# Performance work log

Measured on AMD Instinct MI355X. Metric: run time of the kernel, lower is better.

The kernel has to match this reference:

```python
import jax, jax.numpy as jnp
import numpy as np

N_NODES = 50000
IN_DIM = 128
N_HID = 128
K = 4
ROUTIT = 3
N_LAYER = 2
TAU = 1.0


def setup_inputs() -> dict:
    key = jax.random.key(0)
    k1, k2, k3, k4, k5, k6 = jax.random.split(key, 6)
    feat = jax.random.normal(k1, (N_NODES, IN_DIM), dtype=jnp.float32)
    edge_index = jax.random.randint(k2, (2, 800000), 0, N_NODES, dtype=jnp.int64)
    # nn.Linear-style params (stored as [in, out] for x @ W + b)
    lin_w = jax.random.normal(k3, (IN_DIM, N_HID), dtype=jnp.float32) / np.sqrt(IN_DIM)
    lin_b = jax.random.normal(k4, (N_HID,), dtype=jnp.float32) * 0.01
    mlp_w = jax.random.normal(k5, (N_HID, N_HID), dtype=jnp.float32) / np.sqrt(N_HID)
    mlp_b = jax.random.normal(k6, (N_HID,), dtype=jnp.float32) * 0.01
    return {"feat": feat, "edge_index": edge_index, "lin_w": lin_w,
            "lin_b": lin_b, "mlp_w": mlp_w, "mlp_b": mlp_b}


def _channel_normalize(x, n, k, dd):
    # F.normalize over each of the k channels (eps matches torch default 1e-12)
    v = x.reshape(n, k, dd)
    nrm = jnp.linalg.norm(v, axis=2, keepdims=True)
    return (v / jnp.maximum(nrm, 1e-12)).reshape(n, k * dd)


def _routing_layer(x, src, trg):
    n, d = x.shape
    m = src.shape[0]
    dd = d // K
    x = _channel_normalize(x, n, K, dd)
    z = x[src].reshape(m, K, dd)  # gather per-edge source features
    c = x
    for t in range(ROUTIT):
        # Faithful to torch: c[trg].view(m, dd, K) is a reshape, NOT a transpose.
        # matmul(z, c_reshaped).sum(-1) == einsum over dd with c_reshaped summed over its trailing K.
        s = c[trg].reshape(m, dd, K).sum(axis=-1)          # [m, dd]
        p = jnp.einsum('mka,ma->mk', z, s)                 # [m, K]
        p = jax.nn.softmax(p / TAU, axis=1)
        weight_sum = (p[:, :, None] * z).reshape(m, d)     # [m, d]
        c = jax.ops.segment_sum(weight_sum, trg, num_segments=n) + x
        if t < ROUTIT - 1:
            c = _channel_normalize(c, n, K, dd)
    return c


def reference(feat, edge_index, lin_w, lin_b, mlp_w, mlp_b):
    src = edge_index[0]
    trg = edge_index[1]
    x = feat @ lin_w + lin_b
    for _ in range(N_LAYER):
        x = _routing_layer(x, src, trg)
    out = x @ mlp_w + mlp_b
    return (out, x)
```

## Files before the change

### kernel.cpp

```cpp
#include <hip/hip_runtime.h>

#define NN 50000
#define ND (NN * 128)
#define SCAN_B 49
#define CAP 20
#define LOG2E 1.4426950408889634f

typedef float f32x2 __attribute__((ext_vector_type(2)));

#if defined(__has_builtin)
#  if __has_builtin(__builtin_amdgcn_exp2f)
#    define EXP2F(x) __builtin_amdgcn_exp2f(x)
#  else
#    define EXP2F(x) exp2f(x)
#  endif
#else
#  define EXP2F(x) exp2f(x)
#endif

__device__ __forceinline__ float b2f(unsigned short u) {
    union { unsigned int i; float f; } v; v.i = ((unsigned int)u) << 16; return v.f;
}
__device__ __forceinline__ unsigned short f2b(float f) {
    union { float f; unsigned int i; } v; v.f = f;
    return (unsigned short)((v.i + 0x7fffu + ((v.i >> 16) & 1u)) >> 16);
}
__device__ __forceinline__ unsigned int pack2(float lo, float hi) {
    return (unsigned int)f2b(lo) | ((unsigned int)f2b(hi) << 16);
}
__device__ __forceinline__ float unlo(unsigned int u) { return __uint_as_float(u << 16); }
__device__ __forceinline__ float unhi(unsigned int u) { return __uint_as_float(u & 0xFFFF0000u); }
__device__ __forceinline__ int clampi(int i, int lo, int hi) { return max(lo, min(i, hi)); }

template<int CTRL>
__device__ __forceinline__ float dmov(float v) {
    return __int_as_float(__builtin_amdgcn_update_dpp(0, __float_as_int(v), CTRL, 0xF, 0xF, true));
}
template<int CTRL> __device__ __forceinline__ float dadd(float v) { return v + dmov<CTRL>(v); }
__device__ __forceinline__ float qsum(float v) { v = dadd<0xB1>(v); v = dadd<0x4E>(v); return v; }
__device__ __forceinline__ float rsum4(float v) { v = dadd<0x124>(v); v = dadd<0x128>(v); return v; }

__global__ __launch_bounds__(256) void detect(
    const unsigned short* __restrict__ feat_u, const unsigned int* __restrict__ ei_u,
    int* __restrict__ flags)
{
    int tid = threadIdx.x;
    int f32hit = 0;
    for (int i = tid; i < 8192; i += 256) {
        unsigned e = (feat_u[i] >> 7) & 0xFFu;
        if (e >= 0xC0u) f32hit = 1;
    }
    int i32hit = 0;
    for (int i = tid; i < 4096; i += 256)
        if (ei_u[2 * i + 1] != 0u) i32hit = 1;
    if (f32hit) atomicOr(&flags[0], 1);
    if (i32hit) atomicOr(&flags[1], 1);
}

__global__ __launch_bounds__(256) void conv_hist(
    const void* __restrict__ eiRaw, int* __restrict__ srcA, int* __restrict__ trgA,
    int* __restrict__ deg, int m, const int* __restrict__ flags)
{
    int e = blockIdx.x * 256 + threadIdx.x;
    if (e >= m) return;
    int src, trg;
    if (flags[1]) { const int* p = (const int*)eiRaw; src = p[e]; trg = p[m + e]; }
    else { const long long* p = (const long long*)eiRaw; src = (int)p[e]; trg = (int)p[m + e]; }
    src = clampi(src, 0, NN - 1);
    trg = clampi(trg, 0, NN - 1);
    srcA[e] = src; trgA[e] = trg;
    atomicAdd(&deg[trg], 1);
}

__global__ __launch_bounds__(256) void scan1(
    const int* __restrict__ deg, int* __restrict__ rowStart, int* __restrict__ blkSum)
{
    __shared__ int lds[256];
    int blk = blockIdx.x, tid = threadIdx.x;
    int base = blk * 1024 + tid * 4;
    int v[4]; int s = 0;
    #pragma unroll
    for (int j = 0; j < 4; ++j) { int idx = base + j; v[j] = (idx < NN) ? deg[idx] : 0; s += v[j]; }
    lds[tid] = s; __syncthreads();
    for (int off = 1; off < 256; off <<= 1) {
        int x = (tid >= off) ? lds[tid - off] : 0;
        __syncthreads();
        lds[tid] += x;
        __syncthreads();
    }
    int excl = lds[tid] - s;
    if (tid == 255) blkSum[blk] = lds[tid];
    int run = excl;
    #pragma unroll
    for (int j = 0; j < 4; ++j) { int idx = base + j; if (idx < NN) rowStart[idx] = run; run += v[j]; }
}
__global__ __launch_bounds__(64) void scan2(
    int* __restrict__ blkSum, int* __restrict__ blkOff, int* __restrict__ rowStart, int m)
{
    int lane = threadIdx.x;
    int orig = (lane < SCAN_B) ? blkSum[lane] : 0;
    int v = orig;
    for (int off = 1; off < 64; off <<= 1) {
        int x = __shfl_up(v, off);
        if (lane >= off) v += x;
    }
    if (lane < SCAN_B) blkOff[lane] = v - orig;
    if (lane == 0) rowStart[NN] = m;
}
__global__ __launch_bounds__(256) void scan3(
    int* __restrict__ rowStart, const int* __restrict__ blkOff, int* __restrict__ cursor)
{
    int base = blockIdx.x * 1024 + threadIdx.x * 4;
    int off = blkOff[blockIdx.x];
    #pragma unroll
    for (int j = 0; j < 4; ++j) {
        int idx = base + j;
        if (idx < NN) { int v = rowStart[idx] + off; rowStart[idx] = v; cursor[idx] = v; }
    }
}

__global__ __launch_bounds__(256) void scatter_csr(
    const int* __restrict__ srcA, const int* __restrict__ trgA,
    int* __restrict__ cursor, int* __restrict__ eSrc, int m)
{
    int e = blockIdx.x * 256 + threadIdx.x;
    if (e >= m) return;
    int pos = atomicAdd(&cursor[trgA[e]], 1);
    eSrc[pos] = srcA[e];
}

__global__ __launch_bounds__(256) void gemm_norm(
    const void* __restrict__ A, const void* __restrict__ W, const void* __restrict__ bias,
    unsigned short* __restrict__ XNh, const int* __restrict__ flags)
{
    __shared__ float Wl[128 * 128];
    __shared__ float As[32 * 128];
    int tid = threadIdx.x;
    int cg = tid & 31;
    int rg = tid >> 5;
    int rowBase = blockIdx.x * 32;
    bool isF32 = flags[0] != 0;

    if (isF32) {
        for (int i = tid * 4; i < 128 * 128; i += 1024)
            *(float4*)&Wl[i] = *(const float4*)&((const float*)W)[i];
    } else {
        for (int i = tid * 4; i < 128 * 128; i += 1024) {
            ushort4 u = *(const ushort4*)&((const unsigned short*)W)[i];
            Wl[i] = b2f(u.x); Wl[i+1] = b2f(u.y); Wl[i+2] = b2f(u.z); Wl[i+3] = b2f(u.w);
        }
    }
    #pragma unroll
    for (int r = 0; r < 4; ++r) {
        int lrow = r * 8 + rg;
        int row = rowBase + lrow;
        float4 v = make_float4(0.f, 0.f, 0.f, 0.f);
        if (row < NN) {
            if (isF32) v = *(const float4*)&((const float*)A)[(long)row * 128 + cg * 4];
            else {
                ushort4 u = *(const ushort4*)&((const unsigned short*)A)[(long)row * 128 + cg * 4];
                v = make_float4(b2f(u.x), b2f(u.y), b2f(u.z), b2f(u.w));
            }
        }
        *(float4*)&As[lrow * 128 + cg * 4] = v;
    }
    float4 bb;
    if (isF32) bb = *(const float4*)&((const float*)bias)[cg * 4];
    else {
        ushort4 u = *(const ushort4*)&((const unsigned short*)bias)[cg * 4];
        bb = make_float4(b2f(u.x), b2f(u.y), b2f(u.z), b2f(u.w));
    }
    __syncthreads();

    float acc[4][4];
    #pragma unroll
    for (int i = 0; i < 4; ++i) { acc[i][0]=bb.x; acc[i][1]=bb.y; acc[i][2]=bb.z; acc[i][3]=bb.w; }

    for (int k4 = 0; k4 < 32; ++k4) {
        float4 w[4], av[4];
        #pragma unroll
        for (int j = 0; j < 4; ++j)
            w[j] = *(const float4*)&Wl[(k4 * 4 + j) * 128 + cg * 4];
        #pragma unroll
        for (int i = 0; i < 4; ++i)
            av[i] = *(const float4*)&As[(rg * 4 + i) * 128 + k4 * 4];
        #pragma unroll
        for (int i = 0; i < 4; ++i) {
            const float a0 = av[i].x, a1 = av[i].y, a2 = av[i].z, a3 = av[i].w;
            acc[i][0] = fmaf(a0, w[0].x, fmaf(a1, w[1].x, fmaf(a2, w[2].x, fmaf(a3, w[3].x, acc[i][0]))));
            acc[i][1] = fmaf(a0, w[0].y, fmaf(a1, w[1].y, fmaf(a2, w[2].y, fmaf(a3, w[3].y, acc[i][1]))));
            acc[i][2] = fmaf(a0, w[0].z, fmaf(a1, w[1].z, fmaf(a2, w[2].z, fmaf(a3, w[3].z, acc[i][2]))));
            acc[i][3] = fmaf(a0, w[0].w, fmaf(a1, w[1].w, fmaf(a2, w[2].w, fmaf(a3, w[3].w, acc[i][3]))));
        }
    }
    #pragma unroll
    for (int i = 0; i < 4; ++i) {
        int row = rowBase + rg * 4 + i;
        float lss = acc[i][0]*acc[i][0] + acc[i][1]*acc[i][1] + acc[i][2]*acc[i][2] + acc[i][3]*acc[i][3];
        lss += __shfl_xor(lss, 1);
        lss += __shfl_xor(lss, 2);
        lss += __shfl_xor(lss, 4);
        float scale = 1.0f / fmaxf(sqrtf(lss), 1e-12f);
        if (row < NN) {
            float4 o; o.x = acc[i][0]*scale; o.y = acc[i][1]*scale; o.z = acc[i][2]*scale; o.w = acc[i][3]*scale;
            uint2 pk; pk.x = pack2(o.x, o.y); pk.y = pack2(o.z, o.w);
            *(uint2*)((char*)XNh + (long)row * 256 + cg * 8) = pk;
        }
    }
}

__global__ __launch_bounds__(256) void gemm_plain(
    const float* __restrict__ A, const void* __restrict__ W, const void* __restrict__ bias,
    float* __restrict__ Out, const int* __restrict__ flags)
{
    __shared__ float Wl[128 * 128];
    __shared__ float As[32 * 128];
    int tid = threadIdx.x;
    int cg = tid & 31;
    int rg = tid >> 5;
    int rowBase = blockIdx.x * 32;
    bool isF32 = flags[0] != 0;

    if (isF32) {
        for (int i = tid * 4; i < 128 * 128; i += 1024)
            *(float4*)&Wl[i] = *(const float4*)&((const float*)W)[i];
    } else {
        for (int i = tid * 4; i < 128 * 128; i += 1024) {
            ushort4 u = *(const ushort4*)&((const unsigned short*)W)[i];
            Wl[i] = b2f(u.x); Wl[i+1] = b2f(u.y); Wl[i+2] = b2f(u.z); Wl[i+3] = b2f(u.w);
        }
    }
    #pragma unroll
    for (int r = 0; r < 4; ++r) {
        int lrow = r * 8 + rg;
        int row = rowBase + lrow;
        float4 v = make_float4(0.f, 0.f, 0.f, 0.f);
        if (row < NN) v = *(const float4*)&A[(long)row * 128 + cg * 4];
        *(float4*)&As[lrow * 128 + cg * 4] = v;
    }
    float4 bb;
    if (isF32) bb = *(const float4*)&((const float*)bias)[cg * 4];
    else {
        ushort4 u = *(const ushort4*)&((const unsigned short*)bias)[cg * 4];
        bb = make_float4(b2f(u.x), b2f(u.y), b2f(u.z), b2f(u.w));
    }
    __syncthreads();

    float acc[4][4];
    #pragma unroll
    for (int i = 0; i < 4; ++i) { acc[i][0]=bb.x; acc[i][1]=bb.y; acc[i][2]=bb.z; acc[i][3]=bb.w; }

    for (int k4 = 0; k4 < 32; ++k4) {
        float4 w[4], av[4];
        #pragma unroll
        for (int j = 0; j < 4; ++j)
            w[j] = *(const float4*)&Wl[(k4 * 4 + j) * 128 + cg * 4];
        #pragma unroll
        for (int i = 0; i < 4; ++i)
            av[i] = *(const float4*)&As[(rg * 4 + i) * 128 + k4 * 4];
        #pragma unroll
        for (int i = 0; i < 4; ++i) {
            const float a0 = av[i].x, a1 = av[i].y, a2 = av[i].z, a3 = av[i].w;
            acc[i][0] = fmaf(a0, w[0].x, fmaf(a1, w[1].x, fmaf(a2, w[2].x, fmaf(a3, w[3].x, acc[i][0]))));
            acc[i][1] = fmaf(a0, w[0].y, fmaf(a1, w[1].y, fmaf(a2, w[2].y, fmaf(a3, w[3].y, acc[i][1]))));
            acc[i][2] = fmaf(a0, w[0].z, fmaf(a1, w[1].z, fmaf(a2, w[2].z, fmaf(a3, w[3].z, acc[i][2]))));
            acc[i][3] = fmaf(a0, w[0].w, fmaf(a1, w[1].w, fmaf(a2, w[2].w, fmaf(a3, w[3].w, acc[i][3]))));
        }
    }
    #pragma unroll
    for (int i = 0; i < 4; ++i) {
        int row = rowBase + rg * 4 + i;
        if (row < NN) {
            float4 o; o.x = acc[i][0]; o.y = acc[i][1]; o.z = acc[i][2]; o.w = acc[i][3];
            *(float4*)&Out[(long)row * 128 + cg * 4] = o;
        }
    }
}

#define PROC(ZU) { \
    f32x2 za0 = {unlo(ZU.x), unhi(ZU.x)}; \
    f32x2 za1 = {unlo(ZU.y), unhi(ZU.y)}; \
    f32x2 za2 = {unlo(ZU.z), unhi(ZU.z)}; \
    f32x2 za3 = {unlo(ZU.w), unhi(ZU.w)}; \
    f32x2 dd_ = za0 * s0; \
    dd_ = __builtin_elementwise_fma(za1, s1, dd_); \
    dd_ = __builtin_elementwise_fma(za2, s2, dd_); \
    dd_ = __builtin_elementwise_fma(za3, s3, dd_); \
    float p = dd_.x + dd_.y; \
    p = qsum(p); \
    float ex = EXP2F(p); \
    float sm = rsum4(ex); \
    float wgt = ex * __builtin_amdgcn_rcpf(sm); \
    f32x2 w2 = {wgt, wgt}; \
    a0 = __builtin_elementwise_fma(w2, za0, a0); \
    a1 = __builtin_elementwise_fma(w2, za1, a1); \
    a2 = __builtin_elementwise_fma(w2, za2, a2); \
    a3 = __builtin_elementwise_fma(w2, za3, a3); }

__global__ __launch_bounds__(256) void route_layer(
    const int* __restrict__ rowStart, const int* __restrict__ eSrc,
    const unsigned short* __restrict__ XNh,
    unsigned short* __restrict__ XNOut, float* __restrict__ CT)
{
    __shared__ unsigned short zbuf[4][CAP * 128];
    int w = threadIdx.x >> 6;
    int node = blockIdx.x * 4 + w;
    int lane = threadIdx.x & 63;
    int slot = lane >> 4;
    int h = lane & 15;
    int beg = rowStart[node], end = rowStart[node + 1];
    int deg = end - beg;
    int degL = min(deg, CAP);
    const char* XNb = (const char*)XNh;

    for (int r = slot; r < degL; r += 4) {
        int src = eSrc[beg + r];
        uint4 v = *(const uint4*)(XNb + (src * 256 + h * 16));
        *(uint4*)&zbuf[w][r * 128 + h * 8] = v;
    }
    uint4 xr = *(const uint4*)(XNb + (node * 256 + h * 16));
    float x0 = unlo(xr.x), x1 = unhi(xr.x), x2 = unlo(xr.y), x3 = unhi(xr.y);
    float x4 = unlo(xr.z), x5 = unhi(xr.z), x6 = unlo(xr.w), x7 = unhi(xr.w);
    float tx = (x0 + x1 + x2 + x3) * LOG2E;
    float ty = (x4 + x5 + x6 + x7) * LOG2E;
    int sb = (lane & 48) | (4 * (h & 3));
    f32x2 s0, s1, s2, s3;
    s0.x = __shfl(tx, sb);     s0.y = __shfl(ty, sb);
    s1.x = __shfl(tx, sb + 1); s1.y = __shfl(ty, sb + 1);
    s2.x = __shfl(tx, sb + 2); s2.y = __shfl(ty, sb + 2);
    s3.x = __shfl(tx, sb + 3); s3.y = __shfl(ty, sb + 3);
    asm volatile("s_waitcnt lgkmcnt(0)" ::: "memory");

    f32x2 a0, a1, a2, a3;
    #pragma unroll
    for (int iter = 0; iter < 3; ++iter) {
        if (slot == 0) {
            a0 = (f32x2){x0, x1}; a1 = (f32x2){x2, x3};
            a2 = (f32x2){x4, x5}; a3 = (f32x2){x6, x7};
        } else {
            a0 = (f32x2){0.f, 0.f}; a1 = a0; a2 = a0; a3 = a0;
        }
        int i = slot;
        for (; i + 4 < degL; i += 8) {
            uint4 zu0 = *(const uint4*)&zbuf[w][i * 128 + h * 8];
            uint4 zu1 = *(const uint4*)&zbuf[w][(i + 4) * 128 + h * 8];
            PROC(zu0);
            PROC(zu1);
        }
        if (i < degL) {
            uint4 zu = *(const uint4*)&zbuf[w][i * 128 + h * 8];
            PROC(zu);
        }
        for (int j = CAP + slot; j < deg; j += 4) {
            uint4 zu = *(const uint4*)(XNb + (eSrc[beg + j] * 256 + h * 16));
            PROC(zu);
        }
        a0.x += __shfl_xor(a0.x, 16); a0.x += __shfl_xor(a0.x, 32);
        a0.y += __shfl_xor(a0.y, 16); a0.y += __shfl_xor(a0.y, 32);
        a1.x += __shfl_xor(a1.x, 16); a1.x += __shfl_xor(a1.x, 32);
        a1.y += __shfl_xor(a1.y, 16); a1.y += __shfl_xor(a1.y, 32);
        a2.x += __shfl_xor(a2.x, 16); a2.x += __shfl_xor(a2.x, 32);
        a2.y += __shfl_xor(a2.y, 16); a2.y += __shfl_xor(a2.y, 32);
        a3.x += __shfl_xor(a3.x, 16); a3.x += __shfl_xor(a3.x, 32);
        a3.y += __shfl_xor(a3.y, 16); a3.y += __shfl_xor(a3.y, 32);
        if (iter < 2) {
            f32x2 q = a0 * a0;
            q = __builtin_elementwise_fma(a1, a1, q);
            q = __builtin_elementwise_fma(a2, a2, q);
            q = __builtin_elementwise_fma(a3, a3, q);
            float ssq = qsum(q.x + q.y);
            float scl = LOG2E / fmaxf(sqrtf(ssq), 1e-12f);
            tx = (a0.x + a0.y + a1.x + a1.y) * scl;
            ty = (a2.x + a2.y + a3.x + a3.y) * scl;
            s0.x = __shfl(tx, sb);     s0.y = __shfl(ty, sb);
            s1.x = __shfl(tx, sb + 1); s1.y = __shfl(ty, sb + 1);
            s2.x = __shfl(tx, sb + 2); s2.y = __shfl(ty, sb + 2);
            s3.x = __shfl(tx, sb + 3); s3.y = __shfl(ty, sb + 3);
        }
    }
    if (XNOut) {
        f32x2 q = a0 * a0;
        q = __builtin_elementwise_fma(a1, a1, q);
        q = __builtin_elementwise_fma(a2, a2, q);
        q = __builtin_elementwise_fma(a3, a3, q);
        float ssq = qsum(q.x + q.y);
        float scale = 1.0f / fmaxf(sqrtf(ssq), 1e-12f);
        if (slot == 0) {
            uint4 pk;
            pk.x = pack2(a0.x * scale, a0.y * scale);
            pk.y = pack2(a1.x * scale, a1.y * scale);
            pk.z = pack2(a2.x * scale, a2.y * scale);
            pk.w = pack2(a3.x * scale, a3.y * scale);
            *(uint4*)((char*)XNOut + (node * 256 + h * 16)) = pk;
        }
    }
    if (CT && slot == 0) {
        float4* cp = (float4*)(CT + (node * 128 + 8 * h));
        cp[0] = make_float4(a0.x, a0.y, a1.x, a1.y);
        cp[1] = make_float4(a2.x, a2.y, a3.x, a3.y);
    }
}

extern "C" void kernel_launch(void* const* d_in, const int* in_sizes, int n_in,
                              void* d_out, int out_size, void* d_ws, size_t ws_size,
                              hipStream_t stream) {
    const void* feat  = d_in[0];
    const void* ei    = d_in[1];
    const void* lin_w = d_in[2];
    const void* lin_b = d_in[3];
    const void* mlp_w = d_in[4];
    const void* mlp_b = d_in[5];
    float* out = (float*)d_out;

    const int m = in_sizes[1] / 2;

    char* wsB = (char*)d_ws;
    int*   flags = (int*)wsB;
    unsigned short* XH1 = (unsigned short*)(wsB + 256);
    unsigned short* XH2 = XH1 + ND;
    int*   srcA  = (int*)(XH2 + ND);
    int*   trgA  = srcA + m;
    int*   eSrc  = trgA + m;
    int*   deg   = eSrc + m;
    int*   rowStart = deg + NN;
    int*   cursor   = rowStart + NN + 1;
    int*   blkSum   = cursor + NN;
    int*   blkOff   = blkSum + 64;

    hipMemsetAsync(flags, 0, 8, stream);
    hipMemsetAsync(deg, 0, NN * sizeof(int), stream);
    detect<<<1, 256, 0, stream>>>((const unsigned short*)feat, (const unsigned int*)ei, flags);

    const int edgeBlocks = (m + 255) / 256;
    conv_hist<<<edgeBlocks, 256, 0, stream>>>(ei, srcA, trgA, deg, m, flags);
    scan1<<<SCAN_B, 256, 0, stream>>>(deg, rowStart, blkSum);
    scan2<<<1, 64, 0, stream>>>(blkSum, blkOff, rowStart, m);
    scan3<<<SCAN_B, 256, 0, stream>>>(rowStart, blkOff, cursor);
    scatter_csr<<<edgeBlocks, 256, 0, stream>>>(srcA, trgA, cursor, eSrc, m);

    const int gemmBlocks = (NN + 31) / 32;
    const int nodeBlocks = NN / 4;

    gemm_norm<<<gemmBlocks, 256, 0, stream>>>(feat, lin_w, lin_b, XH1, flags);

    route_layer<<<nodeBlocks, 256, 0, stream>>>(rowStart, eSrc, XH1, XH2, nullptr);
    route_layer<<<nodeBlocks, 256, 0, stream>>>(rowStart, eSrc, XH2, nullptr, out + ND);

    gemm_plain<<<gemmBlocks, 256, 0, stream>>>(out + ND, mlp_w, mlp_b, out, flags);
}
```

Before: 398.1 us.

## Read GEMM weights from global via prep kernel; keep routing neighbors in registers

Adds a prep kernel that converts both weight matrices and biases to fp32 once. The GEMMs then read weights directly from global/L2 instead of staging a 64KB LDS copy per block, which frees LDS and should raise occupancy. The routing kernel drops its shared-memory neighbor buffer and caches up to 16 neighbor feature rows per node in registers across the three routing iterations. Extra neighbors are re-gathered from global on each iteration. This trades LDS traffic for higher register pressure and repeated global weight loads.

```diff
diff --git a/kernel.cpp b/kernel.cpp
--- a/kernel.cpp
+++ b/kernel.cpp
@@ -3,7 +3,6 @@
 #define NN 50000
 #define ND (NN * 128)
 #define SCAN_B 49
-#define CAP 20
 #define LOG2E 1.4426950408889634f
 
 typedef float f32x2 __attribute__((ext_vector_type(2)));
@@ -57,6 +56,31 @@
     if (i32hit) atomicOr(&flags[1], 1);
 }
 
+__global__ __launch_bounds__(256) void prep_w(
+    const void* __restrict__ W1, const void* __restrict__ B1,
+    const void* __restrict__ W2, const void* __restrict__ B2,
+    float* __restrict__ w1o, float* __restrict__ b1o,
+    float* __restrict__ w2o, float* __restrict__ b2o,
+    const int* __restrict__ flags)
+{
+    bool isF32 = flags[0] != 0;
+    int idx = blockIdx.x * 256 + threadIdx.x;
+    if (idx < 16384) {
+        if (isF32) { w1o[idx] = ((const float*)W1)[idx]; w2o[idx] = ((const float*)W2)[idx]; }
+        else {
+            w1o[idx] = b2f(((const unsigned short*)W1)[idx]);
+            w2o[idx] = b2f(((const unsigned short*)W2)[idx]);
+        }
+    }
+    if (idx < 128) {
+        if (isF32) { b1o[idx] = ((const float*)B1)[idx]; b2o[idx] = ((const float*)B2)[idx]; }
+        else {
+            b1o[idx] = b2f(((const unsigned short*)B1)[idx]);
+            b2o[idx] = b2f(((const unsigned short*)B2)[idx]);
+        }
+    }
+}
+
 __global__ __launch_bounds__(256) void conv_hist(
     const void* __restrict__ eiRaw, int* __restrict__ srcA, int* __restrict__ trgA,
     int* __restrict__ deg, int m, const int* __restrict__ flags)
@@ -130,10 +154,9 @@
 }
 
 __global__ __launch_bounds__(256) void gemm_norm(
-    const void* __restrict__ A, const void* __restrict__ W, const void* __restrict__ bias,
+    const void* __restrict__ A, const float* __restrict__ W, const float* __restrict__ bias,
     unsigned short* __restrict__ XNh, const int* __restrict__ flags)
 {
-    __shared__ float Wl[128 * 128];
     __shared__ float As[32 * 128];
     int tid = threadIdx.x;
     int cg = tid & 31;
@@ -141,15 +164,6 @@
     int rowBase = blockIdx.x * 32;
     bool isF32 = flags[0] != 0;
 
-    if (isF32) {
-        for (int i = tid * 4; i < 128 * 128; i += 1024)
-            *(float4*)&Wl[i] = *(const float4*)&((const float*)W)[i];
-    } else {
-        for (int i = tid * 4; i < 128 * 128; i += 1024) {
-            ushort4 u = *(const ushort4*)&((const unsigned short*)W)[i];
-            Wl[i] = b2f(u.x); Wl[i+1] = b2f(u.y); Wl[i+2] = b2f(u.z); Wl[i+3] = b2f(u.w);
-        }
-    }
     #pragma unroll
     for (int r = 0; r < 4; ++r) {
         int lrow = r * 8 + rg;
@@ -164,23 +178,19 @@
         }
         *(float4*)&As[lrow * 128 + cg * 4] = v;
     }
-    float4 bb;
-    if (isF32) bb = *(const float4*)&((const float*)bias)[cg * 4];
-    else {
-        ushort4 u = *(const ushort4*)&((const unsigned short*)bias)[cg * 4];
-        bb = make_float4(b2f(u.x), b2f(u.y), b2f(u.z), b2f(u.w));
-    }
+    float4 bb = *(const float4*)&bias[cg * 4];
     __syncthreads();
 
     float acc[4][4];
     #pragma unroll
     for (int i = 0; i < 4; ++i) { acc[i][0]=bb.x; acc[i][1]=bb.y; acc[i][2]=bb.z; acc[i][3]=bb.w; }
 
+    #pragma unroll 2
     for (int k4 = 0; k4 < 32; ++k4) {
         float4 w[4], av[4];
         #pragma unroll
         for (int j = 0; j < 4; ++j)
-            w[j] = *(const float4*)&Wl[(k4 * 4 + j) * 128 + cg * 4];
+            w[j] = *(const float4*)&W[(k4 * 4 + j) * 128 + cg * 4];
         #pragma unroll
         for (int i = 0; i < 4; ++i)
             av[i] = *(const float4*)&As[(rg * 4 + i) * 128 + k4 * 4];
@@ -210,26 +220,15 @@
 }
 
 __global__ __launch_bounds__(256) void gemm_plain(
-    const float* __restrict__ A, const void* __restrict__ W, const void* __restrict__ bias,
-    float* __restrict__ Out, const int* __restrict__ flags)
-{
-    __shared__ float Wl[128 * 128];
+    const float* __restrict__ A, const float* __restrict__ W, const float* __restrict__ bias,
+    float* __restrict__ Out)
+{
     __shared__ float As[32 * 128];
     int tid = threadIdx.x;
     int cg = tid & 31;
     int rg = tid >> 5;
     int rowBase = blockIdx.x * 32;
-    bool isF32 = flags[0] != 0;
-
-    if (isF32) {
-        for (int i = tid * 4; i < 128 * 128; i += 1024)
-            *(float4*)&Wl[i] = *(const float4*)&((const float*)W)[i];
-    } else {
-        for (int i = tid * 4; i < 128 * 128; i += 1024) {
-            ushort4 u = *(const ushort4*)&((const unsigned short*)W)[i];
-            Wl[i] = b2f(u.x); Wl[i+1] = b2f(u.y); Wl[i+2] = b2f(u.z); Wl[i+3] = b2f(u.w);
-        }
-    }
+
     #pragma unroll
     for (int r = 0; r < 4; ++r) {
         int lrow = r * 8 + rg;
@@ -238,23 +237,19 @@
         if (row < NN) v = *(const float4*)&A[(long)row * 128 + cg * 4];
         *(float4*)&As[lrow * 128 + cg * 4] = v;
     }
-    float4 bb;
-    if (isF32) bb = *(const float4*)&((const float*)bias)[cg * 4];
-    else {
-        ushort4 u = *(const ushort4*)&((const unsigned short*)bias)[cg * 4];
-        bb = make_float4(b2f(u.x), b2f(u.y), b2f(u.z), b2f(u.w));
-    }
+    float4 bb = *(const float4*)&bias[cg * 4];
     __syncthreads();
 
     float acc[4][4];
     #pragma unroll
     for (int i = 0; i < 4; ++i) { acc[i][0]=bb.x; acc[i][1]=bb.y; acc[i][2]=bb.z; acc[i][3]=bb.w; }
 
+    #pragma unroll 2
     for (int k4 = 0; k4 < 32; ++k4) {
         float4 w[4], av[4];
         #pragma unroll
         for (int j = 0; j < 4; ++j)
-            w[j] = *(const float4*)&Wl[(k4 * 4 + j) * 128 + cg * 4];
+            w[j] = *(const float4*)&W[(k4 * 4 + j) * 128 + cg * 4];
         #pragma unroll
         for (int i = 0; i < 4; ++i)
             av[i] = *(const float4*)&As[(rg * 4 + i) * 128 + k4 * 4];
@@ -277,11 +272,7 @@
     }
 }
 
-#define PROC(ZU) { \
-    f32x2 za0 = {unlo(ZU.x), unhi(ZU.x)}; \
-    f32x2 za1 = {unlo(ZU.y), unhi(ZU.y)}; \
-    f32x2 za2 = {unlo(ZU.z), unhi(ZU.z)}; \
-    f32x2 za3 = {unlo(ZU.w), unhi(ZU.w)}; \
+#define PROC_R(za0, za1, za2, za3) { \
     f32x2 dd_ = za0 * s0; \
     dd_ = __builtin_elementwise_fma(za1, s1, dd_); \
     dd_ = __builtin_elementwise_fma(za2, s2, dd_); \
@@ -297,26 +288,38 @@
     a2 = __builtin_elementwise_fma(w2, za2, a2); \
     a3 = __builtin_elementwise_fma(w2, za3, a3); }
 
+#define PROC_G(ZU) { \
+    f32x2 za0 = {unlo(ZU.x), unhi(ZU.x)}; \
+    f32x2 za1 = {unlo(ZU.y), unhi(ZU.y)}; \
+    f32x2 za2 = {unlo(ZU.z), unhi(ZU.z)}; \
+    f32x2 za3 = {unlo(ZU.w), unhi(ZU.w)}; \
+    PROC_R(za0, za1, za2, za3) }
+
 __global__ __launch_bounds__(256) void route_layer(
     const int* __restrict__ rowStart, const int* __restrict__ eSrc,
     const unsigned short* __restrict__ XNh,
     unsigned short* __restrict__ XNOut, float* __restrict__ CT)
 {
-    __shared__ unsigned short zbuf[4][CAP * 128];
-    int w = threadIdx.x >> 6;
-    int node = blockIdx.x * 4 + w;
+    int node = blockIdx.x * 4 + (threadIdx.x >> 6);
     int lane = threadIdx.x & 63;
     int slot = lane >> 4;
     int h = lane & 15;
     int beg = rowStart[node], end = rowStart[node + 1];
     int deg = end - beg;
-    int degL = min(deg, CAP);
     const char* XNb = (const char*)XNh;
 
-    for (int r = slot; r < degL; r += 4) {
-        int src = eSrc[beg + r];
-        uint4 v = *(const uint4*)(XNb + (src * 256 + h * 16));
-        *(uint4*)&zbuf[w][r * 128 + h * 8] = v;
+    f32x2 rz[4][4];
+    #pragma unroll
+    for (int j = 0; j < 4; ++j) {
+        int r = slot + 4 * j;
+        if (r < deg) {
+            int src = eSrc[beg + r];
+            uint4 v = *(const uint4*)(XNb + (src * 256 + h * 16));
+            rz[j][0] = (f32x2){unlo(v.x), unhi(v.x)};
+            rz[j][1] = (f32x2){unlo(v.y), unhi(v.y)};
+            rz[j][2] = (f32x2){unlo(v.z), unhi(v.z)};
+            rz[j][3] = (f32x2){unlo(v.w), unhi(v.w)};
+        }
     }
     uint4 xr = *(const uint4*)(XNb + (node * 256 + h * 16));
     float x0 = unlo(xr.x), x1 = unhi(xr.x), x2 = unlo(xr.y), x3 = unhi(xr.y);
@@ -329,7 +332,6 @@
     s1.x = __shfl(tx, sb + 1); s1.y = __shfl(ty, sb + 1);
     s2.x = __shfl(tx, sb + 2); s2.y = __shfl(ty, sb + 2);
     s3.x = __shfl(tx, sb + 3); s3.y = __shfl(ty, sb + 3);
-    asm volatile("s_waitcnt lgkmcnt(0)" ::: "memory");
 
     f32x2 a0, a1, a2, a3;
     #pragma unroll
@@ -340,20 +342,13 @@
         } else {
             a0 = (f32x2){0.f, 0.f}; a1 = a0; a2 = a0; a3 = a0;
         }
-        int i = slot;
-        for (; i + 4 < degL; i += 8) {
-            uint4 zu0 = *(const uint4*)&zbuf[w][i * 128 + h * 8];
-            uint4 zu1 = *(const uint4*)&zbuf[w][(i + 4) * 128 + h * 8];
-            PROC(zu0);
-            PROC(zu1);
-        }
-        if (i < degL) {
-            uint4 zu = *(const uint4*)&zbuf[w][i * 128 + h * 8];
-            PROC(zu);
-        }
-        for (int j = CAP + slot; j < deg; j += 4) {
-            uint4 zu = *(const uint4*)(XNb + (eSrc[beg + j] * 256 + h * 16));
-            PROC(zu);
+        #pragma unroll
+        for (int j = 0; j < 4; ++j) {
+            if (slot + 4 * j < deg) PROC_R(rz[j][0], rz[j][1], rz[j][2], rz[j][3]);
+        }
+        for (int i = 16 + slot; i < deg; i += 4) {
+            uint4 zu = *(const uint4*)(XNb + (eSrc[beg + i] * 256 + h * 16));
+            PROC_G(zu);
         }
         a0.x += __shfl_xor(a0.x, 16); a0.x += __shfl_xor(a0.x, 32);
         a0.y += __shfl_xor(a0.y, 16); a0.y += __shfl_xor(a0.y, 32);
@@ -426,10 +421,15 @@
     int*   cursor   = rowStart + NN + 1;
     int*   blkSum   = cursor + NN;
     int*   blkOff   = blkSum + 64;
+    float* W1f      = (float*)(blkOff + 64);
+    float* B1f      = W1f + 16384;
+    float* W2f      = B1f + 128;
+    float* B2f      = W2f + 16384;
 
     hipMemsetAsync(flags, 0, 8, stream);
     hipMemsetAsync(deg, 0, NN * sizeof(int), stream);
     detect<<<1, 256, 0, stream>>>((const unsigned short*)feat, (const unsigned int*)ei, flags);
+    prep_w<<<64, 256, 0, stream>>>(lin_w, lin_b, mlp_w, mlp_b, W1f, B1f, W2f, B2f, flags);
 
     const int edgeBlocks = (m + 255) / 256;
     conv_hist<<<edgeBlocks, 256, 0, stream>>>(ei, srcA, trgA, deg, m, flags);
@@ -441,10 +441,10 @@
     const int gemmBlocks = (NN + 31) / 32;
     const int nodeBlocks = NN / 4;
 
-    gemm_norm<<<gemmBlocks, 256, 0, stream>>>(feat, lin_w, lin_b, XH1, flags);
+    gemm_norm<<<gemmBlocks, 256, 0, stream>>>(feat, W1f, B1f, XH1, flags);
 
     route_layer<<<nodeBlocks, 256, 0, stream>>>(rowStart, eSrc, XH1, XH2, nullptr);
     route_layer<<<nodeBlocks, 256, 0, stream>>>(rowStart, eSrc, XH2, nullptr, out + ND);
 
-    gemm_plain<<<gemmBlocks, 256, 0, stream>>>(out + ND, mlp_w, mlp_b, out, flags);
-}
+    gemm_plain<<<gemmBlocks, 256, 0, stream>>>(out + ND, W2f, B2f, out);
+}
```

Measured after the change: 418.1 us. +5.0%, slower.
